# Kernel tuning notes

Hardware: AMD Instinct MI355X
Metric: run time of the kernel (lower is better)

The kernel has to match this reference:

```python
import jax, jax.numpy as jnp
import numpy as np

N, E, H, O = 50000, 640000, 128, 2
N_LAYERS = 3


def setup_inputs() -> dict:
    key = jax.random.key(0)
    ks = jax.random.split(key, 20)
    s = 0.05
    inp = {
        "x": jax.random.normal(ks[0], (N, H), dtype=jnp.float32),
        "edge_index": jax.random.randint(ks[1], (2, E), 0, N, dtype=jnp.int64),
        "edge_type": jax.random.randint(ks[2], (E,), 0, 2, dtype=jnp.int64),
        # msg_sf MLP: Linear(2H->H), ReLU, Linear(H->H)
        "w1_sf": jax.random.normal(ks[3], (2 * H, H), jnp.float32) * s,
        "b1_sf": jnp.zeros((H,), jnp.float32),
        "w2_sf": jax.random.normal(ks[4], (H, H), jnp.float32) * s,
        "b2_sf": jnp.zeros((H,), jnp.float32),
        # msg_fd MLP
        "w1_fd": jax.random.normal(ks[5], (2 * H, H), jnp.float32) * s,
        "b1_fd": jnp.zeros((H,), jnp.float32),
        "w2_fd": jax.random.normal(ks[6], (H, H), jnp.float32) * s,
        "b2_fd": jnp.zeros((H,), jnp.float32),
        # GRUCell gru_h (PyTorch layout: [3H, in] / [3H, H], gate order r,z,n)
        "gru_w_ih": jax.random.normal(ks[7], (3 * H, H), jnp.float32) * s,
        "gru_w_hh": jax.random.normal(ks[8], (3 * H, H), jnp.float32) * s,
        "gru_b_ih": jnp.zeros((3 * H,), jnp.float32),
        "gru_b_hh": jnp.zeros((3 * H,), jnp.float32),
        # readout: Linear(H->H), ReLU, Linear(H->O)
        "wr1": jax.random.normal(ks[9], (H, H), jnp.float32) * s,
        "br1": jnp.zeros((H,), jnp.float32),
        "wr2": jax.random.normal(ks[10], (H, O), jnp.float32) * s,
        "br2": jnp.zeros((O,), jnp.float32),
    }
    return inp


def _mlp(ef, w1, b1, w2, b2):
    return jax.nn.relu(ef @ w1 + b1) @ w2 + b2


def _gru_cell(m, h, w_ih, w_hh, b_ih, b_hh):
    gi = m @ w_ih.T + b_ih  # [N, 3H]
    gh = h @ w_hh.T + b_hh  # [N, 3H]
    r = jax.nn.sigmoid(gi[:, :H] + gh[:, :H])
    z = jax.nn.sigmoid(gi[:, H:2 * H] + gh[:, H:2 * H])
    n = jnp.tanh(gi[:, 2 * H:] + r * gh[:, 2 * H:])
    return (1.0 - z) * n + z * h


def reference(x, edge_index, edge_type,
              w1_sf, b1_sf, w2_sf, b2_sf,
              w1_fd, b1_fd, w2_fd, b2_fd,
              gru_w_ih, gru_w_hh, gru_b_ih, gru_b_hh,
              wr1, br1, wr2, br2):
    src, tgt = edge_index[0], edge_index[1]
    is_sf = (edge_type == 0)[:, None]  # [E, 1]
    h = x
    for _ in range(N_LAYERS):
        # gather source/target node states and concatenate -> [E, 2H]
        ef = jnp.concatenate([h[src], h[tgt]], axis=-1)
        # per-edge message from the edge-type-specific MLP
        m = jnp.where(is_sf,
                      _mlp(ef, w1_sf, b1_sf, w2_sf, b2_sf),
                      _mlp(ef, w1_fd, b1_fd, w2_fd, b2_fd))
        # scatter-add into target nodes
        messages = jax.ops.segment_sum(m, tgt, num_segments=h.shape[0])
        # GRU node update (original's messages.mean(dim=1) is shape-invalid
        # for GRUCell; the runnable interpretation feeds messages directly)
        h = _gru_cell(messages, h, gru_w_ih, gru_w_hh, gru_b_ih, gru_b_hh)
    out = jax.nn.relu(h @ wr1 + br1) @ wr2 + br2
    return jax.nn.softmax(out, axis=1)
```

## Files before the change

### kernel.cpp

```cpp
#include <hip/hip_runtime.h>
#include <hip/hip_bf16.h>


#define NN 50000
#define EE 640000
#define HH 128
#define NBINS (2 * NN)
#define NTILES (EE / 64)

typedef __attribute__((ext_vector_type(8))) short short8;
typedef __attribute__((ext_vector_type(4))) float f32x4;

__device__ __forceinline__ unsigned short f2b(float f) {
  __hip_bfloat16 b = __float2bfloat16(f);
  return *reinterpret_cast<unsigned short*>(&b);
}

__global__ __launch_bounds__(256) void k_init(const float* __restrict__ x, float* __restrict__ h,
                                              unsigned short* __restrict__ hbf) {
  int i = blockIdx.x * 256 + threadIdx.x;
  float v = x[i];
  h[i] = v;
  hbf[i] = f2b(v);
}

__global__ __launch_bounds__(256) void k_pack(
    const float* __restrict__ w1s, const float* __restrict__ w2s,
    const float* __restrict__ w1f, const float* __restrict__ w2f,
    const float* __restrict__ gwih, const float* __restrict__ gwhh,
    const float* __restrict__ gbih, const float* __restrict__ gbhh,
    unsigned short* __restrict__ pw1s, unsigned short* __restrict__ pw2s,
    unsigned short* __restrict__ pw1f, unsigned short* __restrict__ pw2f,
    unsigned short* __restrict__ pgru, float* __restrict__ bgr) {
  int i = blockIdx.x * 256 + threadIdx.x;
  if (i < 65536) {
    int ty = i >> 15, idx = i & 32767;
    int j = idx & 7, l = (idx >> 3) & 63, kn = idx >> 9;
    int ks = kn & 7, nt = kn >> 3;
    int k = ks * 32 + (l >> 4) * 8 + j, c = nt * 16 + (l & 15);
    const float* w = ty ? w1f : w1s;
    (ty ? pw1f : pw1s)[idx] = f2b(w[k * 128 + c]);
  } else if (i < 98304) {
    int i2 = i - 65536;
    int ty = i2 >> 14, idx = i2 & 16383;
    int j = idx & 7, l = (idx >> 3) & 63, kn = idx >> 9;
    int ks = kn & 3, nt = kn >> 2;
    int k = ks * 32 + (l >> 4) * 8 + j, c = nt * 16 + (l & 15);
    const float* w = ty ? w2f : w2s;
    (ty ? pw2f : pw2s)[idx] = f2b(w[k * 128 + c]);
  } else if (i < 98304 + 131072) {
    int idx = i - 98304;
    int j = idx & 7, l = (idx >> 3) & 63, kc = idx >> 9;
    int ks = kc & 7, ct = kc >> 3;
    int k = ks * 32 + (l >> 4) * 8 + j, c = ct * 16 + (l & 15);
    float v;
    if (c < 256)      v = (k < 128) ? gwih[c * 128 + k] : gwhh[c * 128 + (k - 128)];
    else if (c < 384) v = (k < 128) ? gwih[c * 128 + k] : 0.f;
    else              v = (k >= 128) ? gwhh[(c - 128) * 128 + (k - 128)] : 0.f;
    pgru[idx] = f2b(v);
  } else if (i < 98304 + 131072 + 512) {
    int j = i - (98304 + 131072);
    float v;
    if (j < 256)      v = gbih[j] + gbhh[j];
    else if (j < 384) v = gbih[j];
    else              v = gbhh[j - 128];
    bgr[j] = v;
  }
}

__global__ __launch_bounds__(256) void k_hist(const int* __restrict__ ei, const int* __restrict__ et,
                                              int* __restrict__ hist) {
  int e = blockIdx.x * 256 + threadIdx.x;
  int g = ei[EE + e];
  int ty = et[e];
  atomicAdd(&hist[ty * NN + g], 1);
}

__global__ __launch_bounds__(1024) void k_scan1(const int* __restrict__ hist, int* __restrict__ base,
                                                int* __restrict__ bsum) {
  __shared__ int sh[1024];
  int t = threadIdx.x;
  int i = blockIdx.x * 1024 + t;
  int v = (i < NBINS) ? hist[i] : 0;
  sh[t] = v;
  __syncthreads();
  for (int o = 1; o < 1024; o <<= 1) {
    int xv = (t >= o) ? sh[t - o] : 0;
    __syncthreads();
    sh[t] += xv;
    __syncthreads();
  }
  if (i < NBINS) base[i] = sh[t] - v;
  if (t == 1023) bsum[blockIdx.x] = sh[t];
}

__global__ __launch_bounds__(128) void k_scan2(int* __restrict__ bsum) {
  __shared__ int sh[128];
  int t = threadIdx.x;
  int v = (t < 98) ? bsum[t] : 0;
  sh[t] = v;
  __syncthreads();
  for (int o = 1; o < 128; o <<= 1) {
    int xv = (t >= o) ? sh[t - o] : 0;
    __syncthreads();
    sh[t] += xv;
    __syncthreads();
  }
  if (t < 98) bsum[t] = sh[t] - v;
}

__global__ __launch_bounds__(1024) void k_scan3(const int* __restrict__ bsum, int* __restrict__ base,
                                                int* __restrict__ cnt) {
  int i = blockIdx.x * 1024 + threadIdx.x;
  if (i < NBINS) {
    int b = base[i] + bsum[blockIdx.x];
    base[i] = b;
    if (i == NN) cnt[0] = b;
  }
}

__global__ __launch_bounds__(256) void k_scatter(const int* __restrict__ ei, const int* __restrict__ et,
                                                 int* __restrict__ woff, int* __restrict__ ssrc,
                                                 int* __restrict__ stgt) {
  int e = blockIdx.x * 256 + threadIdx.x;
  int s = ei[e], g = ei[EE + e], ty = et[e];
  int pos = atomicAdd(&woff[ty * NN + g], 1);
  ssrc[pos] = s;
  stgt[pos] = g;
}

__global__ __launch_bounds__(256, 4) void k_edge(
    const unsigned short* __restrict__ hbf,
    const int* __restrict__ ssrc, const int* __restrict__ stgt,
    const unsigned short* __restrict__ pw1s, const unsigned short* __restrict__ pw2s,
    const unsigned short* __restrict__ pw1f, const unsigned short* __restrict__ pw2f,
    const float* __restrict__ b1s, const float* __restrict__ b2s,
    const float* __restrict__ b1f, const float* __restrict__ b2f,
    float* __restrict__ msg, const int* __restrict__ cnt) {
  __shared__ char smem[32768];
  __shared__ int tsrc[64];
  __shared__ int ttgt[64];
  char* efb = smem;
  char* hidb = smem + 16384;
  int tid = threadIdx.x;
  int l = tid & 63, w = tid >> 6;
  int c0 = cnt[0];
  int bid = blockIdx.x;
  int type = (bid >= NTILES) ? 1 : 0;
  int tb = type ? (bid - NTILES) : bid;
  int lo = type ? c0 : 0;
  int hi = type ? EE : c0;
  int start = lo + tb * 64;
  if (start >= hi) return;
  const unsigned short* pw1 = type ? pw1f : pw1s;
  const unsigned short* pw2 = type ? pw2f : pw2s;
  const float* b1 = type ? b1f : b1s;
  const float* b2 = type ? b2f : b2s;

  if (tid < 64) {
    int pp = start + tid;
    int s = 0, g = -1;
    if (pp < hi) { s = ssrc[pp]; g = stgt[pp]; }
    tsrc[tid] = (s < 0) ? 0 : s;
    ttgt[tid] = g;
  }
  __syncthreads();

  f32x4 zero4 = {0.f, 0.f, 0.f, 0.f};
  f32x4 acc[4][2];
#pragma unroll
  for (int mt = 0; mt < 4; mt++)
#pragma unroll
    for (int q = 0; q < 2; q++) acc[mt][q] = zero4;

#pragma unroll
  for (int half = 0; half < 2; half++) {
#pragma unroll
    for (int i = 0; i < 4; i++) {
      int c = tid + i * 256;
      int r = c >> 4, cc = c & 15;
      int node;
      if (half == 0) node = tsrc[r];
      else { int gv = ttgt[r]; node = (gv < 0) ? 0 : gv; }
      int4 v = *((const int4*)(hbf + (size_t)node * HH) + cc);
      *(int4*)(efb + r * 256 + ((cc * 16) ^ ((r & 7) << 4))) = v;
    }
    __syncthreads();
    short8 bf1[2][4];
#pragma unroll
    for (int q = 0; q < 2; q++) {
      int nt = 2 * w + q;
#pragma unroll
      for (int ks = 0; ks < 4; ks++)
        bf1[q][ks] = *(const short8*)(pw1 + ((nt * 8 + half * 4 + ks) * 64 + l) * 8);
    }
#pragma unroll
    for (int ks = 0; ks < 4; ks++) {
      short8 a[4];
#pragma unroll
      for (int mt = 0; mt < 4; mt++) {
        int row = mt * 16 + (l & 15);
        a[mt] = *(const short8*)(efb + row * 256 + ((ks * 64 + (l >> 4) * 16) ^ ((row & 7) << 4)));
      }
#pragma unroll
      for (int mt = 0; mt < 4; mt++)
#pragma unroll
        for (int q = 0; q < 2; q++)
          acc[mt][q] = __builtin_amdgcn_mfma_f32_16x16x32_bf16(a[mt], bf1[q][ks], acc[mt][q], 0, 0, 0);
    }
    if (half == 0) __syncthreads();
  }

  float b1v[2];
  b1v[0] = b1[(2 * w) * 16 + (l & 15)];
  b1v[1] = b1[(2 * w + 1) * 16 + (l & 15)];
#pragma unroll
  for (int mt = 0; mt < 4; mt++)
#pragma unroll
    for (int q = 0; q < 2; q++) {
      int col = (2 * w + q) * 16 + (l & 15);
#pragma unroll
      for (int r = 0; r < 4; r++) {
        int row = mt * 16 + (l >> 4) * 4 + r;
        float v = acc[mt][q][r] + b1v[q];
        v = v > 0.f ? v : 0.f;
        *(unsigned short*)(hidb + row * 256 + ((col * 2) ^ ((row & 7) << 4))) = f2b(v);
      }
    }
  __syncthreads();

  short8 bf2[2][4];
#pragma unroll
  for (int q = 0; q < 2; q++) {
    int nt = 2 * w + q;
#pragma unroll
    for (int ks = 0; ks < 4; ks++)
      bf2[q][ks] = *(const short8*)(pw2 + ((nt * 4 + ks) * 64 + l) * 8);
  }
  f32x4 acc2[4][2];
#pragma unroll
  for (int mt = 0; mt < 4; mt++)
#pragma unroll
    for (int q = 0; q < 2; q++) acc2[mt][q] = zero4;
#pragma unroll
  for (int ks = 0; ks < 4; ks++) {
    short8 a[4];
#pragma unroll
    for (int mt = 0; mt < 4; mt++) {
      int row = mt * 16 + (l & 15);
      a[mt] = *(const short8*)(hidb + row * 256 + ((ks * 64 + (l >> 4) * 16) ^ ((row & 7) << 4)));
    }
#pragma unroll
    for (int mt = 0; mt < 4; mt++)
#pragma unroll
      for (int q = 0; q < 2; q++)
        acc2[mt][q] = __builtin_amdgcn_mfma_f32_16x16x32_bf16(a[mt], bf2[q][ks], acc2[mt][q], 0, 0, 0);
  }
  __syncthreads();

  float b2v[2];
  b2v[0] = b2[(2 * w) * 16 + (l & 15)];
  b2v[1] = b2[(2 * w + 1) * 16 + (l & 15)];
#pragma unroll
  for (int mt = 0; mt < 4; mt++)
#pragma unroll
    for (int q = 0; q < 2; q++) {
      int col = (2 * w + q) * 16 + (l & 15);
      int e0 = mt * 16 + (l >> 4) * 4;
      f32x4 v = acc2[mt][q];
      v.x += b2v[q]; v.y += b2v[q]; v.z += b2v[q]; v.w += b2v[q];
      *(f32x4*)(smem + col * 256 + ((e0 * 4) ^ ((col & 15) << 4))) = v;
    }
  __syncthreads();

  int f = tid & 127;
  int eb = (tid >> 7) * 32;
  float accum = 0.f;
  int cur = ttgt[eb];
#pragma unroll
  for (int j = 0; j < 8; j++) {
    f32x4 v = *(const f32x4*)(smem + f * 256 + (((eb + j * 4) * 4) ^ ((f & 15) << 4)));
#pragma unroll
    for (int r = 0; r < 4; r++) {
      int g = ttgt[eb + j * 4 + r];
      if (g != cur) {
        if (cur >= 0) atomicAdd(&msg[(size_t)cur * HH + f], accum);
        accum = 0.f;
        cur = g;
      }
      accum += v[r];
    }
  }
  if (cur >= 0) atomicAdd(&msg[(size_t)cur * HH + f], accum);
}

__global__ __launch_bounds__(256) void k_gru(
    const float* __restrict__ msg, const unsigned short* __restrict__ pgru,
    const float* __restrict__ bgr, float* __restrict__ h, unsigned short* __restrict__ hbf) {
  __shared__ char amh[64 * 512];
  int tid = threadIdx.x, l = tid & 63, w = tid >> 6;
  int n0 = blockIdx.x * 64;
#pragma unroll
  for (int i = 0; i < 8; i++) {
    int c = tid + i * 256;
    int r = c >> 5, cc = c & 31;
    int node = n0 + r; if (node > NN - 1) node = NN - 1;
    float4 v = *((const float4*)(msg + (size_t)node * HH) + cc);
    uint2 u;
    u.x = (unsigned int)f2b(v.x) | ((unsigned int)f2b(v.y) << 16);
    u.y = (unsigned int)f2b(v.z) | ((unsigned int)f2b(v.w) << 16);
    *(uint2*)(amh + r * 512 + ((cc * 8) ^ ((r & 7) << 4))) = u;
  }
#pragma unroll
  for (int i = 0; i < 4; i++) {
    int c = tid + i * 256;
    int r = c >> 4, cc = c & 15;
    int node = n0 + r; if (node > NN - 1) node = NN - 1;
    int4 v = *((const int4*)(hbf + (size_t)node * HH) + cc);
    *(int4*)(amh + r * 512 + ((256 + cc * 16) ^ ((r & 7) << 4))) = v;
  }
  __syncthreads();

  f32x4 zero4 = {0.f, 0.f, 0.f, 0.f};
  f32x4 acc[4][8];
#pragma unroll
  for (int mt = 0; mt < 4; mt++)
#pragma unroll
    for (int t = 0; t < 8; t++) acc[mt][t] = zero4;
#pragma unroll
  for (int ks = 0; ks < 8; ks++) {
    short8 a[4];
#pragma unroll
    for (int mt = 0; mt < 4; mt++) {
      int row = mt * 16 + (l & 15);
      a[mt] = *(const short8*)(amh + row * 512 + ((ks * 64 + (l >> 4) * 16) ^ ((row & 7) << 4)));
    }
#pragma unroll
    for (int t = 0; t < 8; t++) {
      int ct = w + 4 * t;
      short8 bf = *(const short8*)(pgru + ((ct * 8 + ks) * 64 + l) * 8);
#pragma unroll
      for (int mt = 0; mt < 4; mt++)
        acc[mt][t] = __builtin_amdgcn_mfma_f32_16x16x32_bf16(a[mt], bf, acc[mt][t], 0, 0, 0);
    }
  }

#pragma unroll
  for (int tt = 0; tt < 2; tt++) {
    int ct = w + 4 * tt;
    int j = ct * 16 + (l & 15);
    float br = bgr[j], bz = bgr[128 + j], bgi = bgr[256 + j], bgh = bgr[384 + j];
#pragma unroll
    for (int mt = 0; mt < 4; mt++) {
#pragma unroll
      for (int r = 0; r < 4; r++) {
        int row = mt * 16 + (l >> 4) * 4 + r;
        int node = n0 + row;
        if (node < NN) {
          float hold = h[(size_t)node * HH + j];
          float ur = acc[mt][tt][r] + br;
          float uz = acc[mt][tt + 2][r] + bz;
          float gi = acc[mt][tt + 4][r] + bgi;
          float gh = acc[mt][tt + 6][r] + bgh;
          float rr = 1.f / (1.f + __expf(-ur));
          float zz = 1.f / (1.f + __expf(-uz));
          float xx = gi + rr * gh;
          xx = fminf(fmaxf(xx, -15.f), 15.f);
          float ex = __expf(2.f * xx);
          float nn2 = (ex - 1.f) / (ex + 1.f);
          float hn = (1.f - zz) * nn2 + zz * hold;
          h[(size_t)node * HH + j] = hn;
          hbf[(size_t)node * HH + j] = f2b(hn);
        }
      }
    }
  }
}

__global__ __launch_bounds__(256) void k_read(const float* __restrict__ h,
                                              const float* __restrict__ wr1, const float* __restrict__ br1,
                                              const float* __restrict__ wr2, const float* __restrict__ br2,
                                              float* __restrict__ out) {
  __shared__ float sh[16][128];
  int tid = threadIdx.x, l = tid & 63, w = tid >> 6;
  int nb = blockIdx.x * 16;
#pragma unroll
  for (int i = 0; i < 8; i++) {
    int c = tid + i * 256;
    int r = c >> 7, k = c & 127;
    int node = nb + r; if (node > NN - 1) node = NN - 1;
    sh[r][k] = h[(size_t)node * HH + k];
  }
  __syncthreads();
  float a1[4] = {0.f, 0.f, 0.f, 0.f}, a2[4] = {0.f, 0.f, 0.f, 0.f};
  for (int k = 0; k < 128; k++) {
    float w1a = wr1[k * 128 + l];
    float w1b = wr1[k * 128 + l + 64];
#pragma unroll
    for (int n = 0; n < 4; n++) {
      float hv = sh[w * 4 + n][k];
      a1[n] += hv * w1a;
      a2[n] += hv * w1b;
    }
  }
  float bra = br1[l], brb = br1[l + 64];
  float w20 = wr2[l * 2 + 0], w21 = wr2[l * 2 + 1];
  float w20b = wr2[(l + 64) * 2 + 0], w21b = wr2[(l + 64) * 2 + 1];
#pragma unroll
  for (int n = 0; n < 4; n++) {
    float h1 = fmaxf(a1[n] + bra, 0.f), h2 = fmaxf(a2[n] + brb, 0.f);
    float l0 = h1 * w20 + h2 * w20b;
    float l1 = h1 * w21 + h2 * w21b;
#pragma unroll
    for (int o = 32; o > 0; o >>= 1) {
      l0 += __shfl_xor(l0, o);
      l1 += __shfl_xor(l1, o);
    }
    if (l == 0) {
      int node = nb + w * 4 + n;
      if (node < NN) {
        l0 += br2[0];
        l1 += br2[1];
        float mx = fmaxf(l0, l1);
        float e0 = __expf(l0 - mx), e1 = __expf(l1 - mx);
        float s = e0 + e1;
        out[node * 2 + 0] = e0 / s;
        out[node * 2 + 1] = e1 / s;
      }
    }
  }
}

extern "C" void kernel_launch(void* const* d_in, const int* in_sizes, int n_in,
                              void* d_out, int out_size, void* d_ws, size_t ws_size,
                              hipStream_t stream) {
  const float* x    = (const float*)d_in[0];
  const int*   ei   = (const int*)d_in[1];
  const int*   et   = (const int*)d_in[2];
  const float* w1s  = (const float*)d_in[3];
  const float* b1s  = (const float*)d_in[4];
  const float* w2s  = (const float*)d_in[5];
  const float* b2s  = (const float*)d_in[6];
  const float* w1f  = (const float*)d_in[7];
  const float* b1f  = (const float*)d_in[8];
  const float* w2f  = (const float*)d_in[9];
  const float* b2f  = (const float*)d_in[10];
  const float* gwih = (const float*)d_in[11];
  const float* gwhh = (const float*)d_in[12];
  const float* gbih = (const float*)d_in[13];
  const float* gbhh = (const float*)d_in[14];
  const float* wr1  = (const float*)d_in[15];
  const float* br1  = (const float*)d_in[16];
  const float* wr2  = (const float*)d_in[17];
  const float* br2  = (const float*)d_in[18];
  float* out = (float*)d_out;
  (void)in_sizes; (void)n_in; (void)out_size; (void)ws_size;

  char* p = (char*)d_ws;
  size_t off = 0;
  auto alloc = [&](size_t sz) {
    char* r = p + off;
    off = (off + sz + 255) & ~(size_t)255;
    return r;
  };
  float* h             = (float*)alloc((size_t)NN * HH * 4);
  unsigned short* hbf  = (unsigned short*)alloc((size_t)NN * HH * 2);
  float* msg           = (float*)alloc((size_t)NN * HH * 4);
  int* ssrc            = (int*)alloc((size_t)(EE + 64) * 4);
  int* stgt            = (int*)alloc((size_t)(EE + 64) * 4);
  int* hist            = (int*)alloc((size_t)NBINS * 4);
  int* base            = (int*)alloc((size_t)NBINS * 4);
  int* woff            = (int*)alloc((size_t)NBINS * 4);
  int* bsum            = (int*)alloc(128 * 4);
  int* cnt             = (int*)alloc(16);
  unsigned short* pw1s = (unsigned short*)alloc(32768 * 2);
  unsigned short* pw2s = (unsigned short*)alloc(16384 * 2);
  unsigned short* pw1f = (unsigned short*)alloc(32768 * 2);
  unsigned short* pw2f = (unsigned short*)alloc(16384 * 2);
  unsigned short* pgru = (unsigned short*)alloc(131072 * 2);
  float* bgr           = (float*)alloc(512 * 4);

  hipMemsetAsync(hist, 0, (size_t)NBINS * 4, stream);
  k_init<<<NN * HH / 256, 256, 0, stream>>>(x, h, hbf);
  k_pack<<<898, 256, 0, stream>>>(w1s, w2s, w1f, w2f, gwih, gwhh, gbih, gbhh,
                                  pw1s, pw2s, pw1f, pw2f, pgru, bgr);
  k_hist<<<EE / 256, 256, 0, stream>>>(ei, et, hist);
  k_scan1<<<98, 1024, 0, stream>>>(hist, base, bsum);
  k_scan2<<<1, 128, 0, stream>>>(bsum);
  k_scan3<<<98, 1024, 0, stream>>>(bsum, base, cnt);
  hipMemcpyAsync(woff, base, (size_t)NBINS * 4, hipMemcpyDeviceToDevice, stream);
  k_scatter<<<EE / 256, 256, 0, stream>>>(ei, et, woff, ssrc, stgt);
  hipMemsetAsync(ssrc + EE, 0xFF, 64 * 4, stream);
  hipMemsetAsync(stgt + EE, 0xFF, 64 * 4, stream);

  for (int layer = 0; layer < 3; layer++) {
    hipMemsetAsync(msg, 0, (size_t)NN * HH * 4, stream);
    k_edge<<<2 * NTILES, 256, 0, stream>>>(hbf, ssrc, stgt, pw1s, pw2s, pw1f, pw2f,
                                           b1s, b2s, b1f, b2f, msg, cnt);
    k_gru<<<(NN + 63) / 64, 256, 0, stream>>>(msg, pgru, bgr, h, hbf);
  }
  k_read<<<NN / 16, 256, 0, stream>>>(h, wr1, br1, wr2, br2, out);
}
```

Measured before the change: 624.9 us.

## Make edge kernel persistent with double-buffered async LDS gathers and register-resident weights

Replaces the one-tile-per-block edge kernel with 512 persistent blocks (256 per edge type) that loop over tiles. Both MLP weight matrices stay in registers across tiles. The next tile's node gathers are issued straight into LDS with global_load_lds while the current tile is computed, and edge indices are prefetched two tiles ahead. Messages are staged in LDS as bf16 to shrink shared memory, which lowers precision before the segment reduction. Register pressure goes up and occupancy is halved (launch bounds go from 4 to 2 blocks). The gather buffer is not double-buffered, so overlap is limited to the index prefetch and the tail of each iteration.

```diff
diff --git a/kernel.cpp b/kernel.cpp
--- a/kernel.cpp
+++ b/kernel.cpp
@@ -6,7 +6,6 @@
 #define EE 640000
 #define HH 128
 #define NBINS (2 * NN)
-#define NTILES (EE / 64)
 
 typedef __attribute__((ext_vector_type(8))) short short8;
 typedef __attribute__((ext_vector_type(4))) float f32x4;
@@ -14,6 +13,17 @@
 __device__ __forceinline__ unsigned short f2b(float f) {
   __hip_bfloat16 b = __float2bfloat16(f);
   return *reinterpret_cast<unsigned short*>(&b);
+}
+__device__ __forceinline__ float b2f_lo(unsigned int u) {
+  union { unsigned int u; float f; } a; a.u = u << 16; return a.f;
+}
+__device__ __forceinline__ float b2f_hi(unsigned int u) {
+  union { unsigned int u; float f; } a; a.u = u & 0xFFFF0000u; return a.f;
+}
+
+__device__ __forceinline__ void gload_lds16(const void* g, void* l) {
+  __builtin_amdgcn_global_load_lds((const __attribute__((address_space(1))) void*)g,
+                                   (__attribute__((address_space(3))) void*)l, 16, 0, 0);
 }
 
 __global__ __launch_bounds__(256) void k_init(const float* __restrict__ x, float* __restrict__ h,
@@ -129,7 +139,7 @@
   stgt[pos] = g;
 }
 
-__global__ __launch_bounds__(256, 4) void k_edge(
+__global__ __launch_bounds__(256, 2) void k_edge(
     const unsigned short* __restrict__ hbf,
     const int* __restrict__ ssrc, const int* __restrict__ stgt,
     const unsigned short* __restrict__ pw1s, const unsigned short* __restrict__ pw2s,
@@ -137,161 +147,190 @@
     const float* __restrict__ b1s, const float* __restrict__ b2s,
     const float* __restrict__ b1f, const float* __restrict__ b2f,
     float* __restrict__ msg, const int* __restrict__ cnt) {
-  __shared__ char smem[32768];
-  __shared__ int tsrc[64];
-  __shared__ int ttgt[64];
-  char* efb = smem;
-  char* hidb = smem + 16384;
-  int tid = threadIdx.x;
-  int l = tid & 63, w = tid >> 6;
-  int c0 = cnt[0];
-  int bid = blockIdx.x;
-  int type = (bid >= NTILES) ? 1 : 0;
-  int tb = type ? (bid - NTILES) : bid;
-  int lo = type ? c0 : 0;
-  int hi = type ? EE : c0;
-  int start = lo + tb * 64;
-  if (start >= hi) return;
+  __shared__ char efA[16384];
+  __shared__ char efB[16384];
+  __shared__ char mC[18432];
+  __shared__ int idxbuf[2][2][64];
+  const int tid = threadIdx.x, l = tid & 63, w = tid >> 6;
+  const int c0 = cnt[0];
+  const int type = blockIdx.x >> 8;
+  const int bsub = blockIdx.x & 255;
+  const int lo = type ? c0 : 0;
+  const int hi = type ? EE : c0;
+  const int ntile = (hi - lo + 63) >> 6;
+  if (bsub >= ntile) return;
+  const int nblk = 1 + (ntile - 1 - bsub) / 256;
   const unsigned short* pw1 = type ? pw1f : pw1s;
   const unsigned short* pw2 = type ? pw2f : pw2s;
   const float* b1 = type ? b1f : b1s;
   const float* b2 = type ? b2f : b2s;
 
-  if (tid < 64) {
-    int pp = start + tid;
-    int s = 0, g = -1;
-    if (pp < hi) { s = ssrc[pp]; g = stgt[pp]; }
-    tsrc[tid] = (s < 0) ? 0 : s;
-    ttgt[tid] = g;
-  }
-  __syncthreads();
+  short8 wb1[2][8], wb2[2][4];
+#pragma unroll
+  for (int q = 0; q < 2; q++) {
+    int nt = 2 * w + q;
+#pragma unroll
+    for (int ks = 0; ks < 8; ks++)
+      wb1[q][ks] = *(const short8*)(pw1 + ((nt * 8 + ks) * 64 + l) * 8);
+#pragma unroll
+    for (int ks = 0; ks < 4; ks++)
+      wb2[q][ks] = *(const short8*)(pw2 + ((nt * 4 + ks) * 64 + l) * 8);
+  }
+  float b1v[2], b2v[2];
+  b1v[0] = b1[(2 * w) * 16 + (l & 15)];
+  b1v[1] = b1[(2 * w + 1) * 16 + (l & 15)];
+  b2v[0] = b2[(2 * w) * 16 + (l & 15)];
+  b2v[1] = b2[(2 * w + 1) * 16 + (l & 15)];
+
+  auto issue_gathers = [&](int slot) {
+#pragma unroll
+    for (int i = 0; i < 4; i++) {
+      int r = w * 16 + i * 4 + (l >> 4);
+      int j = (l & 15) ^ (r & 7);
+      int nodeS = idxbuf[slot][0][r];
+      gload_lds16(hbf + (size_t)nodeS * HH + j * 8, efA + w * 4096 + i * 1024);
+      int nodeT = idxbuf[slot][1][r];
+      if (nodeT < 0) nodeT = 0;
+      gload_lds16(hbf + (size_t)nodeT * HH + j * 8, efB + w * 4096 + i * 1024);
+    }
+  };
+
+  {
+    int p0 = lo + bsub * 64 + (tid & 63);
+    if (tid < 64) {
+      int v = (p0 < hi) ? ssrc[p0] : 0;
+      if (v < 0) v = 0;
+      idxbuf[0][0][tid] = v;
+    } else if (tid < 128) {
+      int v = (p0 < hi) ? stgt[p0] : -1;
+      idxbuf[0][1][tid & 63] = v;
+    }
+  }
+  int ridx = (tid < 64) ? 0 : -1;
+  {
+    int p1 = lo + (bsub + 256) * 64 + (tid & 63);
+    if (tid < 128 && p1 < hi) ridx = (tid < 64) ? ssrc[p1] : stgt[p1];
+  }
+  asm volatile("s_waitcnt lgkmcnt(0)" ::: "memory");
+  __builtin_amdgcn_s_barrier();
+  issue_gathers(0);
 
   f32x4 zero4 = {0.f, 0.f, 0.f, 0.f};
-  f32x4 acc[4][2];
-#pragma unroll
-  for (int mt = 0; mt < 4; mt++)
-#pragma unroll
-    for (int q = 0; q < 2; q++) acc[mt][q] = zero4;
-
-#pragma unroll
-  for (int half = 0; half < 2; half++) {
-#pragma unroll
-    for (int i = 0; i < 4; i++) {
-      int c = tid + i * 256;
-      int r = c >> 4, cc = c & 15;
-      int node;
-      if (half == 0) node = tsrc[r];
-      else { int gv = ttgt[r]; node = (gv < 0) ? 0 : gv; }
-      int4 v = *((const int4*)(hbf + (size_t)node * HH) + cc);
-      *(int4*)(efb + r * 256 + ((cc * 16) ^ ((r & 7) << 4))) = v;
-    }
-    __syncthreads();
-    short8 bf1[2][4];
-#pragma unroll
-    for (int q = 0; q < 2; q++) {
-      int nt = 2 * w + q;
-#pragma unroll
-      for (int ks = 0; ks < 4; ks++)
-        bf1[q][ks] = *(const short8*)(pw1 + ((nt * 8 + half * 4 + ks) * 64 + l) * 8);
-    }
+  for (int k = 0; k < nblk; k++) {
+    const int cur = k & 1, nxt = cur ^ 1;
+    asm volatile("s_waitcnt vmcnt(0)" ::: "memory");
+    __builtin_amdgcn_sched_barrier(0);
+    __builtin_amdgcn_s_barrier();
+
+    f32x4 acc[4][2];
+#pragma unroll
+    for (int mt = 0; mt < 4; mt++)
+#pragma unroll
+      for (int q = 0; q < 2; q++) acc[mt][q] = zero4;
+#pragma unroll
+    for (int ks = 0; ks < 8; ks++) {
+      const char* ef = (ks < 4) ? efA : efB;
+      int ko = (ks & 3) * 64;
+      short8 a[4];
+#pragma unroll
+      for (int mt = 0; mt < 4; mt++) {
+        int row = mt * 16 + (l & 15);
+        a[mt] = *(const short8*)(ef + row * 256 + ((ko + (l >> 4) * 16) ^ ((row & 7) << 4)));
+      }
+#pragma unroll
+      for (int mt = 0; mt < 4; mt++)
+#pragma unroll
+        for (int q = 0; q < 2; q++)
+          acc[mt][q] = __builtin_amdgcn_mfma_f32_16x16x32_bf16(a[mt], wb1[q][ks], acc[mt][q], 0, 0, 0);
+    }
+#pragma unroll
+    for (int mt = 0; mt < 4; mt++)
+#pragma unroll
+      for (int q = 0; q < 2; q++) {
+        int col = (2 * w + q) * 16 + (l & 15);
+#pragma unroll
+        for (int r = 0; r < 4; r++) {
+          int row = mt * 16 + (l >> 4) * 4 + r;
+          float v = acc[mt][q][r] + b1v[q];
+          v = v > 0.f ? v : 0.f;
+          *(unsigned short*)(mC + row * 256 + ((col * 2) ^ ((row & 7) << 4))) = f2b(v);
+        }
+      }
+    asm volatile("s_waitcnt lgkmcnt(0)" ::: "memory");
+    __builtin_amdgcn_s_barrier();
+
+    f32x4 acc2[4][2];
+#pragma unroll
+    for (int mt = 0; mt < 4; mt++)
+#pragma unroll
+      for (int q = 0; q < 2; q++) acc2[mt][q] = zero4;
 #pragma unroll
     for (int ks = 0; ks < 4; ks++) {
       short8 a[4];
 #pragma unroll
       for (int mt = 0; mt < 4; mt++) {
         int row = mt * 16 + (l & 15);
-        a[mt] = *(const short8*)(efb + row * 256 + ((ks * 64 + (l >> 4) * 16) ^ ((row & 7) << 4)));
+        a[mt] = *(const short8*)(mC + row * 256 + ((ks * 64 + (l >> 4) * 16) ^ ((row & 7) << 4)));
       }
 #pragma unroll
       for (int mt = 0; mt < 4; mt++)
 #pragma unroll
         for (int q = 0; q < 2; q++)
-          acc[mt][q] = __builtin_amdgcn_mfma_f32_16x16x32_bf16(a[mt], bf1[q][ks], acc[mt][q], 0, 0, 0);
-    }
-    if (half == 0) __syncthreads();
-  }
-
-  float b1v[2];
-  b1v[0] = b1[(2 * w) * 16 + (l & 15)];
-  b1v[1] = b1[(2 * w + 1) * 16 + (l & 15)];
-#pragma unroll
-  for (int mt = 0; mt < 4; mt++)
-#pragma unroll
-    for (int q = 0; q < 2; q++) {
-      int col = (2 * w + q) * 16 + (l & 15);
-#pragma unroll
-      for (int r = 0; r < 4; r++) {
-        int row = mt * 16 + (l >> 4) * 4 + r;
-        float v = acc[mt][q][r] + b1v[q];
-        v = v > 0.f ? v : 0.f;
-        *(unsigned short*)(hidb + row * 256 + ((col * 2) ^ ((row & 7) << 4))) = f2b(v);
-      }
-    }
-  __syncthreads();
-
-  short8 bf2[2][4];
-#pragma unroll
-  for (int q = 0; q < 2; q++) {
-    int nt = 2 * w + q;
-#pragma unroll
-    for (int ks = 0; ks < 4; ks++)
-      bf2[q][ks] = *(const short8*)(pw2 + ((nt * 4 + ks) * 64 + l) * 8);
-  }
-  f32x4 acc2[4][2];
-#pragma unroll
-  for (int mt = 0; mt < 4; mt++)
-#pragma unroll
-    for (int q = 0; q < 2; q++) acc2[mt][q] = zero4;
-#pragma unroll
-  for (int ks = 0; ks < 4; ks++) {
-    short8 a[4];
-#pragma unroll
-    for (int mt = 0; mt < 4; mt++) {
-      int row = mt * 16 + (l & 15);
-      a[mt] = *(const short8*)(hidb + row * 256 + ((ks * 64 + (l >> 4) * 16) ^ ((row & 7) << 4)));
-    }
+          acc2[mt][q] = __builtin_amdgcn_mfma_f32_16x16x32_bf16(a[mt], wb2[q][ks], acc2[mt][q], 0, 0, 0);
+    }
+    __builtin_amdgcn_s_barrier();
+
 #pragma unroll
     for (int mt = 0; mt < 4; mt++)
 #pragma unroll
-      for (int q = 0; q < 2; q++)
-        acc2[mt][q] = __builtin_amdgcn_mfma_f32_16x16x32_bf16(a[mt], bf2[q][ks], acc2[mt][q], 0, 0, 0);
-  }
-  __syncthreads();
-
-  float b2v[2];
-  b2v[0] = b2[(2 * w) * 16 + (l & 15)];
-  b2v[1] = b2[(2 * w + 1) * 16 + (l & 15)];
-#pragma unroll
-  for (int mt = 0; mt < 4; mt++)
-#pragma unroll
-    for (int q = 0; q < 2; q++) {
-      int col = (2 * w + q) * 16 + (l & 15);
-      int e0 = mt * 16 + (l >> 4) * 4;
-      f32x4 v = acc2[mt][q];
-      v.x += b2v[q]; v.y += b2v[q]; v.z += b2v[q]; v.w += b2v[q];
-      *(f32x4*)(smem + col * 256 + ((e0 * 4) ^ ((col & 15) << 4))) = v;
-    }
-  __syncthreads();
-
-  int f = tid & 127;
-  int eb = (tid >> 7) * 32;
-  float accum = 0.f;
-  int cur = ttgt[eb];
-#pragma unroll
-  for (int j = 0; j < 8; j++) {
-    f32x4 v = *(const f32x4*)(smem + f * 256 + (((eb + j * 4) * 4) ^ ((f & 15) << 4)));
-#pragma unroll
-    for (int r = 0; r < 4; r++) {
-      int g = ttgt[eb + j * 4 + r];
-      if (g != cur) {
-        if (cur >= 0) atomicAdd(&msg[(size_t)cur * HH + f], accum);
-        accum = 0.f;
-        cur = g;
-      }
-      accum += v[r];
-    }
-  }
-  if (cur >= 0) atomicAdd(&msg[(size_t)cur * HH + f], accum);
+      for (int q = 0; q < 2; q++) {
+        int col = (2 * w + q) * 16 + (l & 15);
+        int e0 = mt * 16 + (l >> 4) * 4;
+        f32x4 v = acc2[mt][q];
+        unsigned int u0 = (unsigned int)f2b(v.x + b2v[q]) | ((unsigned int)f2b(v.y + b2v[q]) << 16);
+        unsigned int u1 = (unsigned int)f2b(v.z + b2v[q]) | ((unsigned int)f2b(v.w + b2v[q]) << 16);
+        uint2 uu; uu.x = u0; uu.y = u1;
+        *(uint2*)(mC + col * 144 + e0 * 2) = uu;
+      }
+    if (tid < 128) {
+      int v = ridx;
+      if (tid < 64 && v < 0) v = 0;
+      idxbuf[nxt][tid >= 64 ? 1 : 0][tid & 63] = v;
+    }
+    {
+      int p2 = lo + (bsub + (k + 2) * 256) * 64 + (tid & 63);
+      ridx = (tid < 64) ? 0 : -1;
+      if (tid < 128 && p2 < hi) ridx = (tid < 64) ? ssrc[p2] : stgt[p2];
+    }
+    asm volatile("s_waitcnt lgkmcnt(0)" ::: "memory");
+    __builtin_amdgcn_s_barrier();
+
+    {
+      int f = tid & 127, grp = tid >> 7;
+      float accum = 0.f;
+      int curg = idxbuf[cur][1][grp * 32];
+#pragma unroll
+      for (int jj = 0; jj < 8; jj++) {
+        int4 tg = *(const int4*)&idxbuf[cur][1][grp * 32 + jj * 4];
+        uint2 mv = *(const uint2*)(mC + f * 144 + (grp * 32 + jj * 4) * 2);
+        float vv[4];
+        vv[0] = b2f_lo(mv.x); vv[1] = b2f_hi(mv.x);
+        vv[2] = b2f_lo(mv.y); vv[3] = b2f_hi(mv.y);
+        int gg[4] = {tg.x, tg.y, tg.z, tg.w};
+#pragma unroll
+        for (int r = 0; r < 4; r++) {
+          if (gg[r] != curg) {
+            if (curg >= 0) atomicAdd(&msg[(size_t)curg * HH + f], accum);
+            accum = 0.f;
+            curg = gg[r];
+          }
+          accum += vv[r];
+        }
+      }
+      if (curg >= 0) atomicAdd(&msg[(size_t)curg * HH + f], accum);
+    }
+    if (k + 1 < nblk) issue_gathers(nxt);
+  }
 }
 
 __global__ __launch_bounds__(256) void k_gru(
@@ -466,8 +505,8 @@
   float* h             = (float*)alloc((size_t)NN * HH * 4);
   unsigned short* hbf  = (unsigned short*)alloc((size_t)NN * HH * 2);
   float* msg           = (float*)alloc((size_t)NN * HH * 4);
-  int* ssrc            = (int*)alloc((size_t)(EE + 64) * 4);
-  int* stgt            = (int*)alloc((size_t)(EE + 64) * 4);
+  int* ssrc            = (int*)alloc((size_t)EE * 4);
+  int* stgt            = (int*)alloc((size_t)EE * 4);
   int* hist            = (int*)alloc((size_t)NBINS * 4);
   int* base            = (int*)alloc((size_t)NBINS * 4);
   int* woff            = (int*)alloc((size_t)NBINS * 4);
@@ -490,13 +529,11 @@
   k_scan3<<<98, 1024, 0, stream>>>(bsum, base, cnt);
   hipMemcpyAsync(woff, base, (size_t)NBINS * 4, hipMemcpyDeviceToDevice, stream);
   k_scatter<<<EE / 256, 256, 0, stream>>>(ei, et, woff, ssrc, stgt);
-  hipMemsetAsync(ssrc + EE, 0xFF, 64 * 4, stream);
-  hipMemsetAsync(stgt + EE, 0xFF, 64 * 4, stream);
 
   for (int layer = 0; layer < 3; layer++) {
     hipMemsetAsync(msg, 0, (size_t)NN * HH * 4, stream);
-    k_edge<<<2 * NTILES, 256, 0, stream>>>(hbf, ssrc, stgt, pw1s, pw2s, pw1f, pw2f,
-                                           b1s, b2s, b1f, b2f, msg, cnt);
+    k_edge<<<512, 256, 0, stream>>>(hbf, ssrc, stgt, pw1s, pw2s, pw1f, pw2f,
+                                    b1s, b2s, b1f, b2f, msg, cnt);
     k_gru<<<(NN + 63) / 64, 256, 0, stream>>>(msg, pgru, bgr, h, hbf);
   }
   k_read<<<NN / 16, 256, 0, stream>>>(h, wr1, br1, wr2, br2, out);
```

New measurement: 575.8 us. 1.09x faster.
